# Kernel optimization log

Measured on AMD Instinct MI355X. Metric: run time of the kernel, lower is better.

The kernel has to match this reference:

```python
import jax, jax.numpy as jnp
import numpy as np

N = 500_000
NX = NY = NZ = 96


def bspline_basis(u):
    # u: [N, 3] in [0,1] -> [N, 3, 4] cubic B-spline basis weights
    u2 = u * u
    u3 = u2 * u
    B0 = (1.0 - 3.0 * u + 3.0 * u2 - u3) / 6.0
    B1 = (4.0 - 6.0 * u2 + 3.0 * u3) / 6.0
    B2 = (1.0 + 3.0 * u + 3.0 * u2 - 3.0 * u3) / 6.0
    B3 = u3 / 6.0
    return jnp.stack([B0, B1, B2, B3], axis=-1)


def setup_inputs() -> dict:
    key = jax.random.key(0)
    k1, k2 = jax.random.split(key)
    verts = jax.random.uniform(k1, (N, 3), dtype=jnp.float32)  # in [0,1)^3
    deltaG = jax.random.normal(k2, (NX, NY, NZ, 3), dtype=jnp.float32) * 0.01
    origin = jnp.zeros((3,), dtype=jnp.float32)
    spacing = jnp.full((3,), 1.0 / NX, dtype=jnp.float32)  # rel spans [0, 96)
    return {"verts": verts, "deltaG": deltaG, "origin": origin, "spacing": spacing}


def reference(verts, deltaG, origin, spacing):
    nx, ny, nz = deltaG.shape[0], deltaG.shape[1], deltaG.shape[2]
    rel = (verts - origin[None, :]) / spacing[None, :]        # [N,3]
    base = jnp.floor(rel)
    u = jnp.clip(rel - base, 0.0, 1.0)
    B = bspline_basis(u)                                      # [N,3,4]

    offs = jnp.arange(4, dtype=jnp.int32)
    idx = (base - 1.0).astype(jnp.int32)[:, :, None] + offs   # [N,3,4]
    ia, ib, ic = idx[:, 0], idx[:, 1], idx[:, 2]              # [N,4] each

    # validity mask for each of the 64 taps
    va = (ia >= 0) & (ia < nx)
    vb = (ib >= 0) & (ib < ny)
    vc = (ic >= 0) & (ic < nz)
    mask = va[:, :, None, None] & vb[:, None, :, None] & vc[:, None, None, :]  # [N,4,4,4]

    # separable tensor-product weights, zeroed for out-of-range taps
    w = B[:, 0, :, None, None] * B[:, 1, None, :, None] * B[:, 2, None, None, :]
    w = jnp.where(mask, w, 0.0)                               # [N,4,4,4]

    flat = (ia[:, :, None, None] * ny + ib[:, None, :, None]) * nz + ic[:, None, None, :]
    flat = jnp.where(mask, flat, 0)                           # safe gather index
    dg = deltaG.reshape(-1, 3)[flat]                          # [N,4,4,4,3]

    out = jnp.einsum('nabc,nabcd->nd', w, dg)                 # [N,3]
    return verts + out
```

## Files before the change

kernel.cpp:

```cpp
#include <hip/hip_runtime.h>
#include <hip/hip_fp16.h>

#define GNX 96
#define GNY 96
#define GNZ 96
#define NBDIM 12
#define NBINS (NBDIM * NBDIM * NBDIM)
#define SUBK 64
#define NKEY (NBINS * SUBK)
#define CAP 64
#define SUP 11
#define SUP3 (SUP * SUP * SUP)
#define NXCD 8

__device__ __forceinline__ int key_of(float vx, float vy, float vz,
                                      float o0, float o1, float o2,
                                      float s0, float s1, float s2,
                                      int copy)
{
    int cx = min(max((int)floorf((vx - o0) / s0), 0), GNX - 1);
    int cy = min(max((int)floorf((vy - o1) / s1), 0), GNY - 1);
    int cz = min(max((int)floorf((vz - o2) / s2), 0), GNZ - 1);
    int coarse = ((cx >> 3) * NBDIM + (cy >> 3)) * NBDIM + (cz >> 3);
    int sub = (((cx >> 2) & 1) << 2) | (((cy >> 2) & 1) << 1) | ((cz >> 2) & 1);
    return (coarse * 8 + sub) * 8 + copy;
}

__global__ __launch_bounds__(256) void zero_kernel(unsigned* __restrict__ counts)
{
    int i = blockIdx.x * 256 + threadIdx.x;
    if (i < NKEY) counts[i] = 0u;
}

__global__ __launch_bounds__(256) void append_kernel(
    const float* __restrict__ verts,
    const float* __restrict__ origin,
    const float* __restrict__ spacing,
    unsigned* __restrict__ counts,
    uint4* __restrict__ slabs, int n)
{
    int i = blockIdx.x * 256 + threadIdx.x;
    if (i >= n) return;
    float vx = verts[3 * i + 0];
    float vy = verts[3 * i + 1];
    float vz = verts[3 * i + 2];
    int key = key_of(vx, vy, vz,
                     origin[0], origin[1], origin[2],
                     spacing[0], spacing[1], spacing[2],
                     blockIdx.x & 7);
    unsigned pos = atomicAdd(&counts[key], 1u);
    if (pos < CAP) {
        uint4 rec;
        rec.x = __float_as_uint(vx);
        rec.y = __float_as_uint(vy);
        rec.z = __float_as_uint(vz);
        rec.w = (unsigned)i;
        slabs[(size_t)key * CAP + pos] = rec;
    }
}

__global__ __launch_bounds__(256) void ffd_bin_kernel(
    const uint4* __restrict__ slabs,
    const unsigned* __restrict__ counts,
    const float* __restrict__ dG,
    const float* __restrict__ origin,
    const float* __restrict__ spacing,
    float* __restrict__ out)
{
    int b = blockIdx.x;
    int bin = (b % NXCD) * (NBINS / NXCD) + b / NXCD;

    int bx = bin / (NBDIM * NBDIM);
    int rem = bin % (NBDIM * NBDIM);
    int by = rem / NBDIM;
    int bz = rem % NBDIM;

    int ox = (bx << 3) - 1;
    int oy = (by << 3) - 1;
    int oz = (bz << 3) - 1;

    __shared__ uint2 s_g[SUP3];
    __shared__ unsigned offs[SUBK + 1];

    if (threadIdx.x < 64) {
        int lane = threadIdx.x;
        unsigned c = min(counts[bin * SUBK + lane], (unsigned)CAP);
        unsigned p = c;
        #pragma unroll
        for (int d = 1; d < 64; d <<= 1) {
            unsigned t = __shfl_up(p, d, 64);
            if (lane >= d) p += t;
        }
        offs[lane + 1] = p;
        if (lane == 0) offs[0] = 0u;
    }

    for (int t = threadIdx.x; t < SUP3; t += 256) {
        int lx = t / (SUP * SUP);
        int r2 = t % (SUP * SUP);
        int ly = r2 / SUP;
        int lz = r2 % SUP;
        int gx = ox + lx, gy = oy + ly, gz = oz + lz;
        uint2 pk = make_uint2(0u, 0u);
        if ((unsigned)gx < GNX && (unsigned)gy < GNY && (unsigned)gz < GNZ) {
            const float* p = dG + 3 * (((gx * GNY) + gy) * GNZ + gz);
            unsigned hx = __half_as_ushort(__float2half(p[0]));
            unsigned hy = __half_as_ushort(__float2half(p[1]));
            unsigned hz = __half_as_ushort(__float2half(p[2]));
            pk.x = hx | (hy << 16);
            pk.y = hz;
        }
        s_g[t] = pk;
    }
    __syncthreads();

    unsigned total = offs[SUBK];

    float o0 = origin[0], o1 = origin[1], o2 = origin[2];
    float sp0 = spacing[0], sp1 = spacing[1], sp2 = spacing[2];

    for (unsigned idx = threadIdx.x; idx < total; idx += 256) {
        int lo = 0, hi = SUBK;
        #pragma unroll
        for (int it = 0; it < 6; ++it) {
            int mid = (lo + hi) >> 1;
            if (offs[mid] <= idx) lo = mid; else hi = mid;
        }
        uint4 rec = slabs[(size_t)(bin * SUBK + lo) * CAP + (idx - offs[lo])];

        float vx = __uint_as_float(rec.x);
        float vy = __uint_as_float(rec.y);
        float vz = __uint_as_float(rec.z);

        float rel[3];
        rel[0] = (vx - o0) / sp0;
        rel[1] = (vy - o1) / sp1;
        rel[2] = (vz - o2) / sp2;
        const int dims[3] = {GNX, GNY, GNZ};
        const int orig3[3] = {ox, oy, oz};

        float B[3][4];
        int   L[3][4];
        #pragma unroll
        for (int d = 0; d < 3; ++d) {
            float fb = floorf(rel[d]);
            float u  = rel[d] - fb;
            u = fminf(fmaxf(u, 0.0f), 1.0f);
            float u2 = u * u;
            float u3 = u2 * u;
            float bb[4];
            bb[0] = (1.0f - 3.0f * u + 3.0f * u2 - u3) * (1.0f / 6.0f);
            bb[1] = (4.0f - 6.0f * u2 + 3.0f * u3) * (1.0f / 6.0f);
            bb[2] = (1.0f + 3.0f * u + 3.0f * u2 - 3.0f * u3) * (1.0f / 6.0f);
            bb[3] = u3 * (1.0f / 6.0f);
            int ib = (int)fb - 1;
            #pragma unroll
            for (int j = 0; j < 4; ++j) {
                int  id    = ib + j;
                bool valid = (id >= 0) && (id < dims[d]);
                B[d][j] = valid ? bb[j] : 0.0f;
                int idc = min(max(id, 0), dims[d] - 1);
                L[d][j] = idc - orig3[d];
            }
        }

        float acc0 = 0.f, acc1 = 0.f, acc2 = 0.f;
        #pragma unroll
        for (int a = 0; a < 4; ++a) {
            float Ba = B[0][a];
            int la = L[0][a] * SUP;
            float sa0 = 0.f, sa1 = 0.f, sa2 = 0.f;
            #pragma unroll
            for (int bq = 0; bq < 4; ++bq) {
                float Bb = B[1][bq];
                int lb = (la + L[1][bq]) * SUP;
                float sb0 = 0.f, sb1 = 0.f, sb2 = 0.f;
                #pragma unroll
                for (int c = 0; c < 4; ++c) {
                    float Bc = B[2][c];
                    uint2 g = s_g[lb + L[2][c]];
                    float gx = __half2float(__ushort_as_half((unsigned short)(g.x & 0xffffu)));
                    float gy = __half2float(__ushort_as_half((unsigned short)(g.x >> 16)));
                    float gz = __half2float(__ushort_as_half((unsigned short)(g.y & 0xffffu)));
                    sb0 = fmaf(Bc, gx, sb0);
                    sb1 = fmaf(Bc, gy, sb1);
                    sb2 = fmaf(Bc, gz, sb2);
                }
                sa0 = fmaf(Bb, sb0, sa0);
                sa1 = fmaf(Bb, sb1, sa1);
                sa2 = fmaf(Bb, sb2, sa2);
            }
            acc0 = fmaf(Ba, sa0, acc0);
            acc1 = fmaf(Ba, sa1, acc1);
            acc2 = fmaf(Ba, sa2, acc2);
        }

        unsigned orig = rec.w;
        out[3 * orig + 0] = vx + acc0;
        out[3 * orig + 1] = vy + acc1;
        out[3 * orig + 2] = vz + acc2;
    }
}

__global__ __launch_bounds__(256) void ffd_direct_kernel(
    const float* __restrict__ verts,
    const float* __restrict__ dG,
    const float* __restrict__ origin,
    const float* __restrict__ spacing,
    float* __restrict__ out, int n)
{
    int i = blockIdx.x * 256 + threadIdx.x;
    if (i >= n) return;
    float vx = verts[3 * i], vy = verts[3 * i + 1], vz = verts[3 * i + 2];
    float rel[3] = {(vx - origin[0]) / spacing[0],
                    (vy - origin[1]) / spacing[1],
                    (vz - origin[2]) / spacing[2]};
    const int dims[3] = {GNX, GNY, GNZ};
    float B[3][4]; int idx[3][4];
    #pragma unroll
    for (int d = 0; d < 3; ++d) {
        float fb = floorf(rel[d]);
        float u = fminf(fmaxf(rel[d] - fb, 0.f), 1.f);
        float u2 = u * u, u3 = u2 * u;
        float bb[4] = {(1.f - 3.f * u + 3.f * u2 - u3) / 6.f,
                       (4.f - 6.f * u2 + 3.f * u3) / 6.f,
                       (1.f + 3.f * u + 3.f * u2 - 3.f * u3) / 6.f,
                       u3 / 6.f};
        int ib = (int)fb - 1;
        #pragma unroll
        for (int j = 0; j < 4; ++j) {
            int id = ib + j;
            bool valid = (id >= 0) && (id < dims[d]);
            B[d][j] = valid ? bb[j] : 0.f;
            idx[d][j] = valid ? id : 0;
        }
    }
    float a0 = 0.f, a1 = 0.f, a2 = 0.f;
    #pragma unroll
    for (int a = 0; a < 4; ++a) {
        float Ba = B[0][a]; int ia = idx[0][a] * GNY;
        float s0 = 0.f, s1 = 0.f, s2 = 0.f;
        #pragma unroll
        for (int bq = 0; bq < 4; ++bq) {
            float Bb = B[1][bq]; int ibb = (ia + idx[1][bq]) * GNZ;
            float t0 = 0.f, t1 = 0.f, t2 = 0.f;
            #pragma unroll
            for (int c = 0; c < 4; ++c) {
                const float* p = dG + 3 * (ibb + idx[2][c]);
                t0 = fmaf(B[2][c], p[0], t0);
                t1 = fmaf(B[2][c], p[1], t1);
                t2 = fmaf(B[2][c], p[2], t2);
            }
            s0 = fmaf(Bb, t0, s0); s1 = fmaf(Bb, t1, s1); s2 = fmaf(Bb, t2, s2);
        }
        a0 = fmaf(Ba, s0, a0); a1 = fmaf(Ba, s1, a1); a2 = fmaf(Ba, s2, a2);
    }
    out[3 * i + 0] = vx + a0;
    out[3 * i + 1] = vy + a1;
    out[3 * i + 2] = vz + a2;
}

extern "C" void kernel_launch(void* const* d_in, const int* in_sizes, int n_in,
                              void* d_out, int out_size, void* d_ws, size_t ws_size,
                              hipStream_t stream) {
    const float* verts   = (const float*)d_in[0];
    const float* dG      = (const float*)d_in[1];
    const float* origin  = (const float*)d_in[2];
    const float* spacing = (const float*)d_in[3];
    float* out = (float*)d_out;

    int n = in_sizes[0] / 3;
    int nblk = (n + 255) / 256;

    size_t countBytes = (size_t)NKEY * sizeof(unsigned);
    size_t slabBytes  = (size_t)NKEY * CAP * sizeof(uint4);
    size_t need = countBytes + slabBytes;

    if (ws_size < need) {
        ffd_direct_kernel<<<nblk, 256, 0, stream>>>(verts, dG, origin, spacing, out, n);
        return;
    }

    unsigned* counts = (unsigned*)d_ws;
    uint4*    slabs  = (uint4*)((char*)d_ws + countBytes);

    zero_kernel<<<(NKEY + 255) / 256, 256, 0, stream>>>(counts);
    append_kernel<<<nblk, 256, 0, stream>>>(verts, origin, spacing, counts, slabs, n);
    ffd_bin_kernel<<<NBINS, 256, 0, stream>>>(slabs, counts, dG, origin, spacing, out);
}
```

Before: 53.07 us.

## Pre-pack grid to fp16 in a separate kernel and widen bin blocks

Adds a pack kernel that converts the whole displacement grid to packed fp16 uint2 once per call. The bin kernel's halo fill then does one 8-byte load per grid point instead of three strided float loads plus conversions. Block size for the bin kernel also goes from 256 to 320 threads. The cost is an extra kernel launch and a full-grid read and write (about 2.6M points), which may outweigh the savings, since halo loads total only about 1728 bins times 1331 points.

Measured after the change: 59.11 us. 1.11x slower.

```diff
diff --git a/kernel.cpp b/kernel.cpp
--- a/kernel.cpp
+++ b/kernel.cpp
@@ -4,6 +4,7 @@
 #define GNX 96
 #define GNY 96
 #define GNZ 96
+#define NPTS (GNX * GNY * GNZ)
 #define NBDIM 12
 #define NBINS (NBDIM * NBDIM * NBDIM)
 #define SUBK 64
@@ -12,6 +13,7 @@
 #define SUP 11
 #define SUP3 (SUP * SUP * SUP)
 #define NXCD 8
+#define FBLK 320
 
 __device__ __forceinline__ int key_of(float vx, float vy, float vz,
                                       float o0, float o1, float o2,
@@ -24,6 +26,26 @@
     int coarse = ((cx >> 3) * NBDIM + (cy >> 3)) * NBDIM + (cz >> 3);
     int sub = (((cx >> 2) & 1) << 2) | (((cy >> 2) & 1) << 1) | ((cz >> 2) & 1);
     return (coarse * 8 + sub) * 8 + copy;
+}
+
+__device__ __forceinline__ float h2f(unsigned u) {
+    return __half2float(__ushort_as_half((unsigned short)(u & 0xffffu)));
+}
+
+__global__ __launch_bounds__(256) void pack_kernel(
+    const float* __restrict__ dG,
+    uint2* __restrict__ dGp)
+{
+    int i = blockIdx.x * 256 + threadIdx.x;
+    if (i >= NPTS) return;
+    float x = dG[3 * i + 0];
+    float y = dG[3 * i + 1];
+    float z = dG[3 * i + 2];
+    uint2 pk;
+    pk.x = (unsigned)__half_as_ushort(__float2half(x))
+         | ((unsigned)__half_as_ushort(__float2half(y)) << 16);
+    pk.y = (unsigned)__half_as_ushort(__float2half(z));
+    dGp[i] = pk;
 }
 
 __global__ __launch_bounds__(256) void zero_kernel(unsigned* __restrict__ counts)
@@ -59,10 +81,10 @@
     }
 }
 
-__global__ __launch_bounds__(256) void ffd_bin_kernel(
+__global__ __launch_bounds__(FBLK) void ffd_bin_kernel(
     const uint4* __restrict__ slabs,
     const unsigned* __restrict__ counts,
-    const float* __restrict__ dG,
+    const uint2* __restrict__ dGp,
     const float* __restrict__ origin,
     const float* __restrict__ spacing,
     float* __restrict__ out)
@@ -95,7 +117,7 @@
         if (lane == 0) offs[0] = 0u;
     }
 
-    for (int t = threadIdx.x; t < SUP3; t += 256) {
+    for (int t = threadIdx.x; t < SUP3; t += FBLK) {
         int lx = t / (SUP * SUP);
         int r2 = t % (SUP * SUP);
         int ly = r2 / SUP;
@@ -103,12 +125,7 @@
         int gx = ox + lx, gy = oy + ly, gz = oz + lz;
         uint2 pk = make_uint2(0u, 0u);
         if ((unsigned)gx < GNX && (unsigned)gy < GNY && (unsigned)gz < GNZ) {
-            const float* p = dG + 3 * (((gx * GNY) + gy) * GNZ + gz);
-            unsigned hx = __half_as_ushort(__float2half(p[0]));
-            unsigned hy = __half_as_ushort(__float2half(p[1]));
-            unsigned hz = __half_as_ushort(__float2half(p[2]));
-            pk.x = hx | (hy << 16);
-            pk.y = hz;
+            pk = dGp[((gx * GNY) + gy) * GNZ + gz];
         }
         s_g[t] = pk;
     }
@@ -119,7 +136,7 @@
     float o0 = origin[0], o1 = origin[1], o2 = origin[2];
     float sp0 = spacing[0], sp1 = spacing[1], sp2 = spacing[2];
 
-    for (unsigned idx = threadIdx.x; idx < total; idx += 256) {
+    for (unsigned idx = threadIdx.x; idx < total; idx += FBLK) {
         int lo = 0, hi = SUBK;
         #pragma unroll
         for (int it = 0; it < 6; ++it) {
@@ -136,7 +153,7 @@
         rel[0] = (vx - o0) / sp0;
         rel[1] = (vy - o1) / sp1;
         rel[2] = (vz - o2) / sp2;
-        const int dims[3] = {GNX, GNY, GNZ};
+        const int dims[3]  = {GNX, GNY, GNZ};
         const int orig3[3] = {ox, oy, oz};
 
         float B[3][4];
@@ -179,9 +196,9 @@
                 for (int c = 0; c < 4; ++c) {
                     float Bc = B[2][c];
                     uint2 g = s_g[lb + L[2][c]];
-                    float gx = __half2float(__ushort_as_half((unsigned short)(g.x & 0xffffu)));
-                    float gy = __half2float(__ushort_as_half((unsigned short)(g.x >> 16)));
-                    float gz = __half2float(__ushort_as_half((unsigned short)(g.y & 0xffffu)));
+                    float gx = h2f(g.x);
+                    float gy = h2f(g.x >> 16);
+                    float gz = h2f(g.y);
                     sb0 = fmaf(Bc, gx, sb0);
                     sb1 = fmaf(Bc, gy, sb1);
                     sb2 = fmaf(Bc, gz, sb2);
@@ -274,7 +291,8 @@
 
     size_t countBytes = (size_t)NKEY * sizeof(unsigned);
     size_t slabBytes  = (size_t)NKEY * CAP * sizeof(uint4);
-    size_t need = countBytes + slabBytes;
+    size_t packBytes  = (size_t)NPTS * sizeof(uint2);
+    size_t need = countBytes + slabBytes + packBytes;
 
     if (ws_size < need) {
         ffd_direct_kernel<<<nblk, 256, 0, stream>>>(verts, dG, origin, spacing, out, n);
@@ -283,8 +301,10 @@
 
     unsigned* counts = (unsigned*)d_ws;
     uint4*    slabs  = (uint4*)((char*)d_ws + countBytes);
-
+    uint2*    dGp    = (uint2*)((char*)d_ws + countBytes + slabBytes);
+
+    pack_kernel<<<(NPTS + 255) / 256, 256, 0, stream>>>(dG, dGp);
     zero_kernel<<<(NKEY + 255) / 256, 256, 0, stream>>>(counts);
     append_kernel<<<nblk, 256, 0, stream>>>(verts, origin, spacing, counts, slabs, n);
-    ffd_bin_kernel<<<NBINS, 256, 0, stream>>>(slabs, counts, dG, origin, spacing, out);
-}
+    ffd_bin_kernel<<<NBINS, FBLK, 0, stream>>>(slabs, counts, dGp, origin, spacing, out);
+}
```
